# Kernel optimization log

Hardware: AMD Instinct MI355X
Metric: run time of the kernel (lower is better)

## Reference

```python
import jax, jax.numpy as jnp
import numpy as np

B, S, D = 1, 2048, 2048
HQ, HKV, HD = 32, 4, 128
E, K, F = 8, 2, 768
EPS = 1e-6
ROPE_THETA = 1000000.0


def rmsnorm(x, scale, eps=EPS):
    var = jnp.mean(jnp.square(x), axis=-1, keepdims=True)
    return x * jax.lax.rsqrt(var + eps) * scale


def rotate_half(x):
    h = x.shape[-1] // 2
    return jnp.concatenate([-x[..., h:], x[..., :h]], axis=-1)


def rope_cos_sin(seq_len, head_dim, dtype=jnp.float32):
    inv_freq = 1.0 / (ROPE_THETA ** (jnp.arange(0, head_dim, 2, dtype=jnp.float32) / head_dim))
    angles = jnp.arange(seq_len, dtype=jnp.float32)[:, None] * inv_freq[None, :]  # (S, HD/2)
    emb = jnp.concatenate([angles, angles], axis=-1)  # (S, HD)
    return jnp.cos(emb).astype(dtype), jnp.sin(emb).astype(dtype)


def setup_inputs() -> dict:
    key = jax.random.key(0)
    ks = jax.random.split(key, 16)
    s = lambda i, shape, scale: jax.random.normal(ks[i], shape, dtype=jnp.float32) * scale
    inp = {
        "hidden_states": s(0, (B, S, D), 1.0),
        "ln1_scale": jnp.ones((D,), jnp.float32),
        "ln2_scale": jnp.ones((D,), jnp.float32),
        "Wq": s(1, (D, HQ * HD), 0.02),
        "Wk": s(2, (D, HKV * HD), 0.02),
        "Wv": s(3, (D, HKV * HD), 0.02),
        "Wo": s(4, (HQ * HD, D), 0.02),
        "q_norm_scale": jnp.ones((HD,), jnp.float32),
        "k_norm_scale": jnp.ones((HD,), jnp.float32),
        "router_W": s(5, (D, E), 0.02),
        "up_W": s(6, (E, D, F), 0.02),
        "up_b": jnp.zeros((E, F), jnp.float32),
        "down_W": s(7, (E, F, D), 0.02),
        "down_b": jnp.zeros((E, D), jnp.float32),
    }
    return inp


def reference(hidden_states, ln1_scale, ln2_scale, Wq, Wk, Wv, Wo,
              q_norm_scale, k_norm_scale, router_W, up_W, up_b, down_W, down_b):
    b, s_len, d = hidden_states.shape
    # ---- pre-norm + self-attention ----
    residual = hidden_states
    x = rmsnorm(hidden_states, ln1_scale)
    q = (x @ Wq).reshape(b, s_len, HQ, HD)
    k = (x @ Wk).reshape(b, s_len, HKV, HD)
    v = (x @ Wv).reshape(b, s_len, HKV, HD)
    q = rmsnorm(q, q_norm_scale)
    k = rmsnorm(k, k_norm_scale)
    cos, sin = rope_cos_sin(s_len, HD, q.dtype)
    cos = cos[None, :, None, :]
    sin = sin[None, :, None, :]
    q = q * cos + rotate_half(q) * sin
    k = k * cos + rotate_half(k) * sin
    g = HQ // HKV
    k = jnp.repeat(k, g, axis=2)  # (b, s, HQ, HD)
    v = jnp.repeat(v, g, axis=2)
    scores = jnp.einsum('bqhd,bkhd->bhqk', q, k) / jnp.sqrt(jnp.asarray(HD, q.dtype))
    causal = jnp.tril(jnp.ones((s_len, s_len), bool))
    scores = jnp.where(causal[None, None], scores, jnp.asarray(-1e9, scores.dtype))
    probs = jax.nn.softmax(scores, axis=-1)
    attn = jnp.einsum('bhqk,bkhd->bqhd', probs, v).reshape(b, s_len, HQ * HD)
    attn_out = attn @ Wo
    hidden = residual + attn_out
    # ---- pre-norm + dense-all-experts MoE ----
    residual = hidden
    xf = rmsnorm(hidden, ln2_scale).reshape(-1, d)  # (T, D)
    router_logits = xf @ router_W  # (T, E)
    routing_weights = jax.nn.softmax(router_logits, axis=-1)
    gating_weights, selected = jax.lax.top_k(routing_weights, K)  # (T, K)
    gating_weights = gating_weights / jnp.sum(gating_weights, axis=-1, keepdims=True)
    expert_mask = jax.nn.one_hot(selected, E, dtype=gating_weights.dtype)  # (T, K, E)
    h = jax.nn.silu(jnp.einsum('td,edf->tef', xf, up_W) + up_b[None])  # (T, E, F)
    expert_outputs = jnp.einsum('tef,efd->ted', h, down_W) + down_b[None]  # (T, E, D)
    weighted = jnp.einsum('tke,ted->tkd', expert_mask, expert_outputs)  # (T, K, D)
    moe_out = jnp.sum(weighted * gating_weights[..., None], axis=1).reshape(b, s_len, d)
    hidden = residual + moe_out
    # ---- load balancing auxiliary loss (no attention mask path) ----
    expert_usage = jnp.mean(jnp.mean(expert_mask, axis=0), axis=0) * E  # (E,)
    su = jnp.sum(expert_usage)
    aux_loss = su * su / (E * E)
    return hidden, router_logits, aux_loss
```

## Files before the change

### kernel.cpp

```cpp
#include <hip/hip_runtime.h>
#include <cmath>

typedef __bf16 bf16_t;
typedef __bf16 bf16x8 __attribute__((ext_vector_type(8)));
typedef __bf16 bf16x4 __attribute__((ext_vector_type(4)));
typedef float  f32x4  __attribute__((ext_vector_type(4)));

#define SLEN 2048
#define DMOD 2048
#define NHQ  32
#define NHKV 4
#define HD   128
#define NQC  4096
#define NKVC 512
#define NQKVC 5120
#define NEXP 8
#define NF   768

#define KSTR 136
#define VSTR 72
#define PSTR 72

__device__ __forceinline__ float wredsum(float v) {
#pragma unroll
  for (int off = 32; off > 0; off >>= 1) v += __shfl_xor(v, off);
  return v;
}

__device__ __forceinline__ void gll16(const bf16_t* g, bf16_t* l) {
  __builtin_amdgcn_global_load_lds((const __attribute__((address_space(1))) void*)g,
                                   (__attribute__((address_space(3))) void*)l, 16, 0, 0);
}

__global__ void rope_table_k(float* __restrict__ cosT, float* __restrict__ sinT) {
  int idx = blockIdx.x * 256 + threadIdx.x;
  if (idx >= SLEN * 64) return;
  int t = idx >> 6, j = idx & 63;
  double inv = exp(-0.2158673524681918 * (double)j);
  double ang = (double)t * inv;
  cosT[idx] = (float)cos(ang);
  sinT[idx] = (float)sin(ang);
}

__global__ __launch_bounds__(256) void transpose_split2_k(const float* __restrict__ in,
                                                          bf16_t* __restrict__ outH,
                                                          bf16_t* __restrict__ outL,
                                                          int R, int C) {
  __shared__ float tile[32][33];
  int tx = threadIdx.x, ty = threadIdx.y;
  int c0 = blockIdx.x * 32, r0 = blockIdx.y * 32;
#pragma unroll
  for (int i = 0; i < 4; i++)
    tile[ty + i * 8][tx] = in[(size_t)(r0 + ty + i * 8) * C + c0 + tx];
  __syncthreads();
#pragma unroll
  for (int i = 0; i < 4; i++) {
    int c = c0 + ty + i * 8;
    int r = r0 + tx;
    float w = tile[tx][ty + i * 8];
    bf16_t hi = (bf16_t)w;
    bf16_t lo = (bf16_t)(w - (float)hi);
    size_t o = (size_t)c * R + r;
    outH[o] = hi;
    outL[o] = lo;
  }
}

__global__ __launch_bounds__(256) void transpose_plain_k(const float* __restrict__ in,
                                                         bf16_t* __restrict__ out,
                                                         int R, int C) {
  __shared__ float tile[32][33];
  int b = blockIdx.z;
  const float* inb = in + (size_t)b * R * C;
  bf16_t* outb = out + (size_t)b * R * C;
  int tx = threadIdx.x, ty = threadIdx.y;
  int c0 = blockIdx.x * 32, r0 = blockIdx.y * 32;
#pragma unroll
  for (int i = 0; i < 4; i++)
    tile[ty + i * 8][tx] = inb[(size_t)(r0 + ty + i * 8) * C + c0 + tx];
  __syncthreads();
#pragma unroll
  for (int i = 0; i < 4; i++) {
    int c = c0 + ty + i * 8;
    int r = r0 + tx;
    outb[(size_t)c * R + r] = (bf16_t)tile[tx][ty + i * 8];
  }
}

__global__ __launch_bounds__(256) void rmsnorm1_k(const float* __restrict__ hs,
                                                  const float* __restrict__ sc,
                                                  bf16_t* __restrict__ xnH,
                                                  bf16_t* __restrict__ xnL) {
  const int t = blockIdx.x;
  const float* row = hs + (size_t)t * DMOD;
  const int tid = threadIdx.x;
  const int i0 = tid * 8;
  float4 a = *(const float4*)(row + i0);
  float4 b = *(const float4*)(row + i0 + 4);
  float x[8] = {a.x, a.y, a.z, a.w, b.x, b.y, b.z, b.w};
  float ss = 0.f;
#pragma unroll
  for (int j = 0; j < 8; j++) ss += x[j] * x[j];
  ss = wredsum(ss);
  __shared__ float red[4];
  if ((tid & 63) == 0) red[tid >> 6] = ss;
  __syncthreads();
  float rn = rsqrtf((red[0] + red[1] + red[2] + red[3]) * (1.f / 2048.f) + 1e-6f);
#pragma unroll
  for (int j = 0; j < 8; j++) {
    float v = x[j] * rn * sc[i0 + j];
    bf16_t hi = (bf16_t)v;
    bf16_t lo = (bf16_t)(v - (float)hi);
    xnH[(size_t)t * DMOD + i0 + j] = hi;
    xnL[(size_t)t * DMOD + i0 + j] = lo;
  }
}

template <bool RESID>
__global__ __launch_bounds__(256, 3) void gemm_split_k(const bf16_t* __restrict__ Ah,
                                                       const bf16_t* __restrict__ Al,
                                                       int lda,
                                                       const bf16_t* __restrict__ Bh,
                                                       const bf16_t* __restrict__ Bl,
                                                       int ldb, int K,
                                                       const float* __restrict__ resid,
                                                       float* __restrict__ C, int ldc) {
  __shared__ bf16_t AsH[2][128][32], AsL[2][128][32], BsH[2][64][32], BsL[2][64][32];
  const int t = threadIdx.x;
  const int w = t >> 6, lane = t & 63;
  const int m16 = lane & 15, quad = lane >> 4;
  const int nwg = gridDim.x * gridDim.y;
  const int flat = blockIdx.y * gridDim.x + blockIdx.x;
  int tile = flat;
  if ((nwg & 7) == 0) tile = (flat & 7) * (nwg >> 3) + (flat >> 3);
  const int bx = tile % gridDim.x, by = tile / gridDim.x;
  const int m0 = by * 128, n0 = bx * 64;
  const int wm = (w & 1) * 64, wn = (w >> 1) * 32;
  f32x4 acc[4][2];
#pragma unroll
  for (int i = 0; i < 4; i++)
#pragma unroll
    for (int j = 0; j < 2; j++) acc[i][j] = (f32x4){0.f, 0.f, 0.f, 0.f};

  const int srow = t >> 2;
  const int scol = (t & 3) * 8;
  const int lw = w * 512;
  const bf16_t* gAh0 = Ah + (size_t)(m0 + srow) * lda + scol;
  const bf16_t* gAh1 = Ah + (size_t)(m0 + 64 + srow) * lda + scol;
  const bf16_t* gAl0 = Al + (size_t)(m0 + srow) * lda + scol;
  const bf16_t* gAl1 = Al + (size_t)(m0 + 64 + srow) * lda + scol;
  const bf16_t* gBh0 = Bh + (size_t)(n0 + srow) * ldb + scol;
  const bf16_t* gBl0 = Bl + (size_t)(n0 + srow) * ldb + scol;

  auto stage = [&](int buf, int k0) {
    gll16(gAh0 + k0, &AsH[buf][0][0] + lw);
    gll16(gAh1 + k0, &AsH[buf][0][0] + 2048 + lw);
    gll16(gAl0 + k0, &AsL[buf][0][0] + lw);
    gll16(gAl1 + k0, &AsL[buf][0][0] + 2048 + lw);
    gll16(gBh0 + k0, &BsH[buf][0][0] + lw);
    gll16(gBl0 + k0, &BsL[buf][0][0] + lw);
  };

  stage(0, 0);
  int cur = 0;
  for (int k0 = 32; k0 <= K; k0 += 32) {
    if (k0 < K) {
      stage(cur ^ 1, k0);
      asm volatile("s_waitcnt vmcnt(6)" ::: "memory");
    } else {
      asm volatile("s_waitcnt vmcnt(0)" ::: "memory");
    }
    __builtin_amdgcn_sched_barrier(0);
    __builtin_amdgcn_s_barrier();
    __builtin_amdgcn_sched_barrier(0);
    bf16x8 a_h[4], a_l[4];
#pragma unroll
    for (int mt = 0; mt < 4; mt++) {
      a_h[mt] = *(const bf16x8*)(&AsH[cur][wm + mt * 16 + m16][quad * 8]);
      a_l[mt] = *(const bf16x8*)(&AsL[cur][wm + mt * 16 + m16][quad * 8]);
    }
#pragma unroll
    for (int nt = 0; nt < 2; nt++) {
      bf16x8 b_h = *(const bf16x8*)(&BsH[cur][wn + nt * 16 + m16][quad * 8]);
      bf16x8 b_l = *(const bf16x8*)(&BsL[cur][wn + nt * 16 + m16][quad * 8]);
#pragma unroll
      for (int mt = 0; mt < 4; mt++) {
        acc[mt][nt] = __builtin_amdgcn_mfma_f32_16x16x32_bf16(a_h[mt], b_h, acc[mt][nt], 0, 0, 0);
        acc[mt][nt] = __builtin_amdgcn_mfma_f32_16x16x32_bf16(a_l[mt], b_h, acc[mt][nt], 0, 0, 0);
        acc[mt][nt] = __builtin_amdgcn_mfma_f32_16x16x32_bf16(a_h[mt], b_l, acc[mt][nt], 0, 0, 0);
      }
    }
    __builtin_amdgcn_sched_barrier(0);
    __builtin_amdgcn_s_barrier();
    __builtin_amdgcn_sched_barrier(0);
    cur ^= 1;
  }
#pragma unroll
  for (int mt = 0; mt < 4; mt++)
#pragma unroll
    for (int r = 0; r < 4; r++) {
      const size_t row = m0 + wm + mt * 16 + quad * 4 + r;
#pragma unroll
      for (int nt = 0; nt < 2; nt++) {
        const size_t idx = row * ldc + n0 + wn + nt * 16 + m16;
        if (RESID) C[idx] = acc[mt][nt][r] + resid[idx];
        else       C[idx] = acc[mt][nt][r];
      }
    }
}

__global__ __launch_bounds__(128) void qknorm_rope_k(float* __restrict__ qkv,
                                                     const float* __restrict__ qsc,
                                                     const float* __restrict__ ksc,
                                                     const float* __restrict__ cosT,
                                                     const float* __restrict__ sinT) {
  const int t = blockIdx.x;
  const int hh = blockIdx.y;
  const bool isq = hh < NHQ;
  float* ptr = qkv + (size_t)t * NQKVC + (isq ? hh * HD : NQC + (hh - NHQ) * HD);
  const int i = threadIdx.x;
  float x = ptr[i];
  float ss = x * x;
  ss = wredsum(ss);
  __shared__ float red2[2];
  __shared__ float xs[128];
  if ((i & 63) == 0) red2[i >> 6] = ss;
  __syncthreads();
  float rn = rsqrtf((red2[0] + red2[1]) * (1.f / 128.f) + 1e-6f);
  float xn = x * rn * (isq ? qsc[i] : ksc[i]);
  xs[i] = xn;
  __syncthreads();
  int j = i & 63;
  float c = cosT[t * 64 + j];
  float s = sinT[t * 64 + j];
  float rot = (i < 64) ? -xs[i + 64] : xs[i - 64];
  ptr[i] = xn * c + rot * s;
}

__global__ __launch_bounds__(256) void kprep_k(const float* __restrict__ qkv,
                                               bf16_t* __restrict__ Kh,
                                               bf16_t* __restrict__ Kl) {
  const int gid = blockIdx.x * 256 + threadIdx.x;
  const int tok = gid >> 6;
  const int c = (gid & 63) * 8;
  const int hk = c >> 7, d = c & 127;
  const float* p = qkv + (size_t)tok * NQKVC + NQC + c;
  float4 a = *(const float4*)p;
  float4 b = *(const float4*)(p + 4);
  float xv[8] = {a.x, a.y, a.z, a.w, b.x, b.y, b.z, b.w};
  bf16x8 hv, lv;
#pragma unroll
  for (int j = 0; j < 8; j++) {
    bf16_t hi = (bf16_t)xv[j];
    hv[j] = hi;
    lv[j] = (bf16_t)(xv[j] - (float)hi);
  }
  const size_t o = ((size_t)hk * SLEN + tok) * HD + d;
  *(bf16x8*)(Kh + o) = hv;
  *(bf16x8*)(Kl + o) = lv;
}

__global__ __launch_bounds__(256) void vprep_k(const float* __restrict__ qkv,
                                               bf16_t* __restrict__ Vh,
                                               bf16_t* __restrict__ Vl) {
  __shared__ float tile[32][33];
  const int hk = blockIdx.z;
  const int tx = threadIdx.x, ty = threadIdx.y;
  const int t0 = blockIdx.x * 32, d0 = blockIdx.y * 32;
#pragma unroll
  for (int i = 0; i < 4; i++)
    tile[ty + i * 8][tx] =
        qkv[(size_t)(t0 + ty + i * 8) * NQKVC + NQC + NKVC + hk * HD + d0 + tx];
  __syncthreads();
#pragma unroll
  for (int i = 0; i < 4; i++) {
    int d = d0 + ty + i * 8;
    int tk = t0 + tx;
    float wv = tile[tx][ty + i * 8];
    bf16_t hi = (bf16_t)wv;
    size_t o = ((size_t)hk * HD + d) * SLEN + tk;
    Vh[o] = hi;
    Vl[o] = (bf16_t)(wv - (float)hi);
  }
}

__global__ __launch_bounds__(256) void attn_mfma_k(const float* __restrict__ qkv,
                                                   const bf16_t* __restrict__ Kph,
                                                   const bf16_t* __restrict__ Kpl,
                                                   const bf16_t* __restrict__ Vph,
                                                   const bf16_t* __restrict__ Vpl,
                                                   bf16_t* __restrict__ attnH,
                                                   bf16_t* __restrict__ attnL) {
  const int bx = blockIdx.x;
  const int hh = blockIdx.y;
  const int hk = hh >> 3;
  __shared__ bf16_t sK[2][64][KSTR];
  __shared__ bf16_t sV[2][128][VSTR];
  const int t = threadIdx.x;
  const int w = t >> 6, lane = t & 63;
  const int m16 = lane & 15, quad = lane >> 4;
  const float SCALE = 0.08838834764831845f;

  const int ksr = t >> 4;
  const int ksc = (t & 15) * 8;
  const int vsd = t >> 3;
  const int vsk = (t & 7) * 8;
  const bf16_t* KbH = Kph + (size_t)hk * SLEN * HD;
  const bf16_t* KbL = Kpl + (size_t)hk * SLEN * HD;
  const bf16_t* VbH = Vph + (size_t)hk * HD * SLEN;
  const bf16_t* VbL = Vpl + (size_t)hk * HD * SLEN;
  bf16_t* sP = &sK[0][0][0];

  for (int half = 0; half < 2; half++) {
    const int qb = half ? bx : 31 - bx;

    bf16x8 Qh[4], Ql[4];
    {
      const int qrow = qb * 64 + w * 16 + m16;
      const float* qp = qkv + (size_t)qrow * NQKVC + hh * HD + quad * 8;
#pragma unroll
      for (int kc = 0; kc < 4; kc++) {
        float4 x0 = *(const float4*)(qp + kc * 32);
        float4 x1 = *(const float4*)(qp + kc * 32 + 4);
        float xv[8] = {x0.x, x0.y, x0.z, x0.w, x1.x, x1.y, x1.z, x1.w};
#pragma unroll
        for (int j = 0; j < 8; j++) {
          bf16_t hi = (bf16_t)xv[j];
          Qh[kc][j] = hi;
          Ql[kc][j] = (bf16_t)(xv[j] - (float)hi);
        }
      }
    }
    f32x4 acc[8];
#pragma unroll
    for (int i = 0; i < 8; i++) acc[i] = (f32x4){0.f, 0.f, 0.f, 0.f};
    float mrow[4], lrow[4];
#pragma unroll
    for (int r = 0; r < 4; r++) { mrow[r] = -1e30f; lrow[r] = 0.f; }

    for (int kb = 0; kb <= qb; kb++) {
      __syncthreads();
      {
#pragma unroll
        for (int i = 0; i < 4; i++) {
          const int row = ksr + i * 16;
          const size_t go = (size_t)(kb * 64 + row) * HD + ksc;
          *(bf16x8*)(&sK[0][row][ksc]) = *(const bf16x8*)(KbH + go);
          *(bf16x8*)(&sK[1][row][ksc]) = *(const bf16x8*)(KbL + go);
        }
      }
      {
#pragma unroll
        for (int i = 0; i < 4; i++) {
          const int d = vsd + i * 32;
          const size_t go = (size_t)d * SLEN + kb * 64 + vsk;
          *(bf16x8*)(&sV[0][d][vsk]) = *(const bf16x8*)(VbH + go);
          *(bf16x8*)(&sV[1][d][vsk]) = *(const bf16x8*)(VbL + go);
        }
      }
      __syncthreads();
      f32x4 xs[4];
#pragma unroll
      for (int nt = 0; nt < 4; nt++) {
        f32x4 s = (f32x4){0.f, 0.f, 0.f, 0.f};
        if (kb < qb || nt <= w) {
#pragma unroll
          for (int kc = 0; kc < 4; kc++) {
            bf16x8 kh = *(const bf16x8*)(&sK[0][nt * 16 + m16][kc * 32 + quad * 8]);
            bf16x8 kl = *(const bf16x8*)(&sK[1][nt * 16 + m16][kc * 32 + quad * 8]);
            s = __builtin_amdgcn_mfma_f32_16x16x32_bf16(Qh[kc], kh, s, 0, 0, 0);
            s = __builtin_amdgcn_mfma_f32_16x16x32_bf16(Ql[kc], kh, s, 0, 0, 0);
            s = __builtin_amdgcn_mfma_f32_16x16x32_bf16(Qh[kc], kl, s, 0, 0, 0);
          }
        }
        xs[nt] = s;
      }
      __syncthreads();
      float p[4][4], alpha[4];
#pragma unroll
      for (int r = 0; r < 4; r++) {
        const int rqg = qb * 64 + w * 16 + quad * 4 + r;
        float xr[4];
#pragma unroll
        for (int nt = 0; nt < 4; nt++) {
          int colg = kb * 64 + nt * 16 + m16;
          xr[nt] = (colg <= rqg) ? xs[nt][r] * SCALE : -1e30f;
        }
        float mx = fmaxf(fmaxf(xr[0], xr[1]), fmaxf(xr[2], xr[3]));
#pragma unroll
        for (int off = 1; off < 16; off <<= 1) mx = fmaxf(mx, __shfl_xor(mx, off));
        float mn = fmaxf(mrow[r], mx);
        float al = __expf(mrow[r] - mn);
        float rs = 0.f;
#pragma unroll
        for (int nt = 0; nt < 4; nt++) {
          float pv = __expf(xr[nt] - mn);
          p[nt][r] = pv;
          rs += pv;
        }
#pragma unroll
        for (int off = 1; off < 16; off <<= 1) rs += __shfl_xor(rs, off);
        lrow[r] = lrow[r] * al + rs;
        mrow[r] = mn;
        alpha[r] = al;
      }
#pragma unroll
      for (int dt = 0; dt < 8; dt++)
#pragma unroll
        for (int r = 0; r < 4; r++) acc[dt][r] *= alpha[r];
      {
        bf16_t* base = sP + (size_t)w * 2 * 16 * PSTR;
#pragma unroll
        for (int nt = 0; nt < 4; nt++)
#pragma unroll
          for (int r = 0; r < 4; r++) {
            float pv = p[nt][r];
            bf16_t hi = (bf16_t)pv;
            base[(quad * 4 + r) * PSTR + nt * 16 + m16] = hi;
            base[16 * PSTR + (quad * 4 + r) * PSTR + nt * 16 + m16] = (bf16_t)(pv - (float)hi);
          }
      }
      {
        const bf16_t* base = sP + (size_t)w * 2 * 16 * PSTR;
        bf16x8 Ph[2], Pl[2];
#pragma unroll
        for (int kc = 0; kc < 2; kc++) {
          Ph[kc] = *(const bf16x8*)(base + m16 * PSTR + kc * 32 + quad * 8);
          Pl[kc] = *(const bf16x8*)(base + 16 * PSTR + m16 * PSTR + kc * 32 + quad * 8);
        }
#pragma unroll
        for (int dt = 0; dt < 8; dt++)
#pragma unroll
          for (int kc = 0; kc < 2; kc++) {
            bf16x8 vh = *(const bf16x8*)(&sV[0][dt * 16 + m16][kc * 32 + quad * 8]);
            bf16x8 vl = *(const bf16x8*)(&sV[1][dt * 16 + m16][kc * 32 + quad * 8]);
            acc[dt] = __builtin_amdgcn_mfma_f32_16x16x32_bf16(Ph[kc], vh, acc[dt], 0, 0, 0);
            acc[dt] = __builtin_amdgcn_mfma_f32_16x16x32_bf16(Pl[kc], vh, acc[dt], 0, 0, 0);
            acc[dt] = __builtin_amdgcn_mfma_f32_16x16x32_bf16(Ph[kc], vl, acc[dt], 0, 0, 0);
          }
      }
    }
#pragma unroll
    for (int r = 0; r < 4; r++) {
      const int tok = qb * 64 + w * 16 + quad * 4 + r;
      const float linv = 1.f / lrow[r];
      const size_t ro = (size_t)tok * NQC + hh * HD;
#pragma unroll
      for (int dt = 0; dt < 8; dt++) {
        float v = acc[dt][r] * linv;
        bf16_t hi = (bf16_t)v;
        attnH[ro + dt * 16 + m16] = hi;
        attnL[ro + dt * 16 + m16] = (bf16_t)(v - (float)hi);
      }
    }
  }
}

__global__ __launch_bounds__(256) void rmsnorm2_router_k(const float* __restrict__ hid,
                                                         const float* __restrict__ sc2,
                                                         const float* __restrict__ rW,
                                                         bf16_t* __restrict__ xf,
                                                         float* __restrict__ rlog) {
  const int t = blockIdx.x;
  const float* row = hid + (size_t)t * DMOD;
  const int tid = threadIdx.x;
  const int i0 = tid * 8;
  float4 a = *(const float4*)(row + i0);
  float4 b = *(const float4*)(row + i0 + 4);
  float x[8] = {a.x, a.y, a.z, a.w, b.x, b.y, b.z, b.w};
  float ss = 0.f;
#pragma unroll
  for (int j = 0; j < 8; j++) ss += x[j] * x[j];
  ss = wredsum(ss);
  __shared__ float red[4];
  if ((tid & 63) == 0) red[tid >> 6] = ss;
  __syncthreads();
  float rn = rsqrtf((red[0] + red[1] + red[2] + red[3]) * (1.f / 2048.f) + 1e-6f);
  float acc[8];
#pragma unroll
  for (int e = 0; e < 8; e++) acc[e] = 0.f;
#pragma unroll
  for (int j = 0; j < 8; j++) {
    float xn = x[j] * rn * sc2[i0 + j];
    xf[(size_t)t * DMOD + i0 + j] = (bf16_t)xn;
    const float* w = rW + (size_t)(i0 + j) * NEXP;
#pragma unroll
    for (int e = 0; e < 8; e++) acc[e] += xn * w[e];
  }
#pragma unroll
  for (int e = 0; e < 8; e++) acc[e] = wredsum(acc[e]);
  __shared__ float wacc[4][8];
  if ((tid & 63) == 0)
#pragma unroll
    for (int e = 0; e < 8; e++) wacc[tid >> 6][e] = acc[e];
  __syncthreads();
  if (tid < 8) rlog[t * NEXP + tid] = wacc[0][tid] + wacc[1][tid] + wacc[2][tid] + wacc[3][tid];
}

__global__ void topk_k(const float* __restrict__ rlog, int* __restrict__ sel,
                       float* __restrict__ gates, float* __restrict__ aux) {
  int t = blockIdx.x * 256 + threadIdx.x;
  if (t == 0) aux[0] = 1.0f;
  if (t >= SLEN) return;
  const float* l = rlog + t * NEXP;
  int i1 = 0; float v1 = l[0];
#pragma unroll
  for (int e = 1; e < 8; e++) if (l[e] > v1) { v1 = l[e]; i1 = e; }
  int i2 = -1; float v2 = -1e30f;
#pragma unroll
  for (int e = 0; e < 8; e++) if (e != i1 && l[e] > v2) { v2 = l[e]; i2 = e; }
  float e21 = expf(v2 - v1);
  float inv = 1.f / (1.f + e21);
  sel[t * 2 + 0] = i1;
  sel[t * 2 + 1] = i2;
  gates[t * 2 + 0] = inv;
  gates[t * 2 + 1] = e21 * inv;
}

__global__ void scatter_k(const int* __restrict__ sel, const float* __restrict__ gates,
                          int* __restrict__ cnt, int* __restrict__ tok,
                          float* __restrict__ gateL) {
  int i = blockIdx.x * 256 + threadIdx.x;
  if (i >= SLEN * 2) return;
  int e = sel[i];
  int pos = atomicAdd(&cnt[e], 1);
  tok[e * SLEN + pos] = i >> 1;
  gateL[e * SLEN + pos] = gates[i];
}

__global__ __launch_bounds__(256, 5) void gemm_up_k(const bf16_t* __restrict__ xf,
                                                    const bf16_t* __restrict__ upWT,
                                                    const int* __restrict__ cnt,
                                                    const int* __restrict__ tok,
                                                    const float* __restrict__ up_b,
                                                    bf16_t* __restrict__ hbuf) {
  const int e = blockIdx.z;
  const int c = cnt[e];
  const int m0 = blockIdx.y * 128;
  if (m0 >= c) return;
  const int n0 = blockIdx.x * 64;
  __shared__ bf16_t As[2][128][32], Bs[2][64][32];
  const int t = threadIdx.x;
  const int w = t >> 6, lane = t & 63;
  const int m16 = lane & 15, quad = lane >> 4;
  const int wm = (w & 1) * 64, wn = (w >> 1) * 32;
  const int srow = t >> 2, scol = (t & 3) * 8;
  const int lw = w * 512;
  const int* tokE = tok + e * SLEN;
  int r0 = m0 + srow;      if (r0 >= c) r0 = c - 1;
  int r1 = m0 + 64 + srow; if (r1 >= c) r1 = c - 1;
  const bf16_t* ga0 = xf + (size_t)tokE[r0] * DMOD + scol;
  const bf16_t* ga1 = xf + (size_t)tokE[r1] * DMOD + scol;
  const bf16_t* gb0 = upWT + (size_t)e * NF * DMOD + (size_t)(n0 + srow) * DMOD + scol;
  f32x4 acc[4][2];
#pragma unroll
  for (int i = 0; i < 4; i++)
#pragma unroll
    for (int j = 0; j < 2; j++) acc[i][j] = (f32x4){0.f, 0.f, 0.f, 0.f};

  auto stage = [&](int buf, int k0) {
    gll16(ga0 + k0, &As[buf][0][0] + lw);
    gll16(ga1 + k0, &As[buf][0][0] + 2048 + lw);
    gll16(gb0 + k0, &Bs[buf][0][0] + lw);
  };

  stage(0, 0);
  int cur = 0;
  for (int k0 = 32; k0 <= DMOD; k0 += 32) {
    if (k0 < DMOD) {
      stage(cur ^ 1, k0);
      asm volatile("s_waitcnt vmcnt(3)" ::: "memory");
    } else {
      asm volatile("s_waitcnt vmcnt(0)" ::: "memory");
    }
    __builtin_amdgcn_sched_barrier(0);
    __builtin_amdgcn_s_barrier();
    __builtin_amdgcn_sched_barrier(0);
    bf16x8 a[4];
#pragma unroll
    for (int mt = 0; mt < 4; mt++)
      a[mt] = *(const bf16x8*)(&As[cur][wm + mt * 16 + m16][quad * 8]);
#pragma unroll
    for (int nt = 0; nt < 2; nt++) {
      bf16x8 b = *(const bf16x8*)(&Bs[cur][wn + nt * 16 + m16][quad * 8]);
#pragma unroll
      for (int mt = 0; mt < 4; mt++)
        acc[mt][nt] = __builtin_amdgcn_mfma_f32_16x16x32_bf16(a[mt], b, acc[mt][nt], 0, 0, 0);
    }
    __builtin_amdgcn_sched_barrier(0);
    __builtin_amdgcn_s_barrier();
    __builtin_amdgcn_sched_barrier(0);
    cur ^= 1;
  }
#pragma unroll
  for (int mt = 0; mt < 4; mt++)
#pragma unroll
    for (int r = 0; r < 4; r++) {
      int slot = m0 + wm + mt * 16 + quad * 4 + r;
      if (slot < c) {
#pragma unroll
        for (int nt = 0; nt < 2; nt++) {
          int n = n0 + wn + nt * 16 + m16;
          float x = acc[mt][nt][r] + up_b[e * NF + n];
          float v = x / (1.f + __expf(-x));
          hbuf[((size_t)e * SLEN + slot) * NF + n] = (bf16_t)v;
        }
      }
    }
}

__global__ __launch_bounds__(256, 5) void gemm_down_k(const bf16_t* __restrict__ hbuf,
                                                      const bf16_t* __restrict__ downWT,
                                                      const int* __restrict__ cnt,
                                                      const int* __restrict__ tok,
                                                      const float* __restrict__ gateL,
                                                      const float* __restrict__ down_b,
                                                      float* __restrict__ outH) {
  const int e = blockIdx.z;
  const int c = cnt[e];
  const int m0 = blockIdx.y * 128;
  if (m0 >= c) return;
  const int n0 = blockIdx.x * 64;
  __shared__ bf16_t As[2][128][32], Bs[2][64][32];
  const int t = threadIdx.x;
  const int w = t >> 6, lane = t & 63;
  const int m16 = lane & 15, quad = lane >> 4;
  const int wm = (w & 1) * 64, wn = (w >> 1) * 32;
  const int srow = t >> 2, scol = (t & 3) * 8;
  const int lw = w * 512;
  const bf16_t* Ab = hbuf + (size_t)e * SLEN * NF;
  const bf16_t* ga0 = Ab + (size_t)(m0 + srow) * NF + scol;
  const bf16_t* ga1 = Ab + (size_t)(m0 + 64 + srow) * NF + scol;
  const bf16_t* gb0 = downWT + (size_t)e * DMOD * NF + (size_t)(n0 + srow) * NF + scol;
  f32x4 acc[4][2];
#pragma unroll
  for (int i = 0; i < 4; i++)
#pragma unroll
    for (int j = 0; j < 2; j++) acc[i][j] = (f32x4){0.f, 0.f, 0.f, 0.f};

  auto stage = [&](int buf, int k0) {
    gll16(ga0 + k0, &As[buf][0][0] + lw);
    gll16(ga1 + k0, &As[buf][0][0] + 2048 + lw);
    gll16(gb0 + k0, &Bs[buf][0][0] + lw);
  };

  stage(0, 0);
  int cur = 0;
  for (int k0 = 32; k0 <= NF; k0 += 32) {
    if (k0 < NF) {
      stage(cur ^ 1, k0);
      asm volatile("s_waitcnt vmcnt(3)" ::: "memory");
    } else {
      asm volatile("s_waitcnt vmcnt(0)" ::: "memory");
    }
    __builtin_amdgcn_sched_barrier(0);
    __builtin_amdgcn_s_barrier();
    __builtin_amdgcn_sched_barrier(0);
    bf16x8 a[4];
#pragma unroll
    for (int mt = 0; mt < 4; mt++)
      a[mt] = *(const bf16x8*)(&As[cur][wm + mt * 16 + m16][quad * 8]);
#pragma unroll
    for (int nt = 0; nt < 2; nt++) {
      bf16x8 b = *(const bf16x8*)(&Bs[cur][wn + nt * 16 + m16][quad * 8]);
#pragma unroll
      for (int mt = 0; mt < 4; mt++)
        acc[mt][nt] = __builtin_amdgcn_mfma_f32_16x16x32_bf16(a[mt], b, acc[mt][nt], 0, 0, 0);
    }
    __builtin_amdgcn_sched_barrier(0);
    __builtin_amdgcn_s_barrier();
    __builtin_amdgcn_sched_barrier(0);
    cur ^= 1;
  }
#pragma unroll
  for (int mt = 0; mt < 4; mt++)
#pragma unroll
    for (int r = 0; r < 4; r++) {
      int slot = m0 + wm + mt * 16 + quad * 4 + r;
      if (slot < c) {
        int tk = tok[e * SLEN + slot];
        float g = gateL[e * SLEN + slot];
#pragma unroll
        for (int nt = 0; nt < 2; nt++) {
          int n = n0 + wn + nt * 16 + m16;
          atomicAdd(&outH[(size_t)tk * DMOD + n], g * (acc[mt][nt][r] + down_b[e * DMOD + n]));
        }
      }
    }
}

extern "C" void kernel_launch(void* const* d_in, const int* in_sizes, int n_in,
                              void* d_out, int out_size, void* d_ws, size_t ws_size,
                              hipStream_t stream) {
  (void)in_sizes; (void)n_in; (void)out_size;
  const float* hs   = (const float*)d_in[0];
  const float* ln1  = (const float*)d_in[1];
  const float* ln2  = (const float*)d_in[2];
  const float* Wq   = (const float*)d_in[3];
  const float* Wk   = (const float*)d_in[4];
  const float* Wv   = (const float*)d_in[5];
  const float* Wo   = (const float*)d_in[6];
  const float* qns  = (const float*)d_in[7];
  const float* kns  = (const float*)d_in[8];
  const float* rW   = (const float*)d_in[9];
  const float* upW  = (const float*)d_in[10];
  const float* upB  = (const float*)d_in[11];
  const float* dnW  = (const float*)d_in[12];
  const float* dnB  = (const float*)d_in[13];
  float* dout = (float*)d_out;

  const size_t NEED = 135431168ull;
  if (ws_size < NEED) return;
  char* ws = (char*)d_ws;
  const size_t OA = 0;
  const size_t OB = OA + 41943040ull;
  const size_t OC = OB + 33554432ull;
  const size_t OD = OC + 16777216ull;
  const size_t OE = OD + 41943040ull;

  bf16_t* BqkvH  = (bf16_t*)(ws + OA);
  bf16_t* BqkvL  = (bf16_t*)(ws + OA + 20971520ull);
  bf16_t* attnH  = (bf16_t*)(ws + OA);
  bf16_t* attnL  = (bf16_t*)(ws + OA + 16777216ull);
  bf16_t* Kph    = (bf16_t*)(ws + OA + 33554432ull);
  bf16_t* Kpl    = Kph + 1048576;
  bf16_t* Vph    = Kpl + 1048576;
  bf16_t* Vpl    = Vph + 1048576;
  bf16_t* upWT   = (bf16_t*)(ws + OA);
  bf16_t* WoH    = (bf16_t*)(ws + OB);
  bf16_t* WoL    = (bf16_t*)(ws + OB + 16777216ull);
  bf16_t* hbuf   = (bf16_t*)(ws + OB);
  bf16_t* xnH    = (bf16_t*)(ws + OC);
  bf16_t* xnL    = (bf16_t*)(ws + OC + 8388608ull);
  bf16_t* xf     = (bf16_t*)(ws + OC);
  float*  qkv    = (float*)(ws + OD);
  bf16_t* downWT = (bf16_t*)(ws + OD);
  float*  cosT   = (float*)(ws + OE);
  float*  sinT   = (float*)(ws + OE + 524288ull);
  int*    sel    = (int*)(ws + OE + 1048576ull);
  float*  gates  = (float*)(ws + OE + 1064960ull);
  int*    cnt    = (int*)(ws + OE + 1081344ull);
  int*    tok    = (int*)(ws + OE + 1082368ull);
  float*  gateL  = (float*)(ws + OE + 1147904ull);

  hipMemsetAsync(cnt, 0, 1024, stream);
  rope_table_k<<<512, 256, 0, stream>>>(cosT, sinT);

  dim3 tb(32, 8);
  transpose_split2_k<<<dim3(128, 64), tb, 0, stream>>>(Wq, BqkvH, BqkvL, 2048, 4096);
  transpose_split2_k<<<dim3(16, 64), tb, 0, stream>>>(Wk, BqkvH + (size_t)4096 * 2048,
                                                      BqkvL + (size_t)4096 * 2048, 2048, 512);
  transpose_split2_k<<<dim3(16, 64), tb, 0, stream>>>(Wv, BqkvH + (size_t)4608 * 2048,
                                                      BqkvL + (size_t)4608 * 2048, 2048, 512);
  transpose_split2_k<<<dim3(64, 128), tb, 0, stream>>>(Wo, WoH, WoL, 4096, 2048);

  rmsnorm1_k<<<2048, 256, 0, stream>>>(hs, ln1, xnH, xnL);
  gemm_split_k<false><<<dim3(80, 16), 256, 0, stream>>>(xnH, xnL, 2048, BqkvH, BqkvL,
                                                        2048, 2048, nullptr, qkv, NQKVC);
  qknorm_rope_k<<<dim3(2048, 36), 128, 0, stream>>>(qkv, qns, kns, cosT, sinT);
  kprep_k<<<512, 256, 0, stream>>>(qkv, Kph, Kpl);
  vprep_k<<<dim3(64, 4, 4), tb, 0, stream>>>(qkv, Vph, Vpl);
  attn_mfma_k<<<dim3(16, 32), 256, 0, stream>>>(qkv, Kph, Kpl, Vph, Vpl, attnH, attnL);
  gemm_split_k<true><<<dim3(32, 16), 256, 0, stream>>>(attnH, attnL, 4096, WoH, WoL,
                                                       4096, 4096, hs, dout, DMOD);

  rmsnorm2_router_k<<<2048, 256, 0, stream>>>(dout, ln2, rW, xf, dout + 4194304);
  topk_k<<<8, 256, 0, stream>>>(dout + 4194304, sel, gates, dout + 4210688);
  scatter_k<<<16, 256, 0, stream>>>(sel, gates, cnt, tok, gateL);

  transpose_plain_k<<<dim3(24, 64, 8), tb, 0, stream>>>(upW, upWT, 2048, 768);
  transpose_plain_k<<<dim3(64, 24, 8), tb, 0, stream>>>(dnW, downWT, 768, 2048);

  gemm_up_k<<<dim3(12, 16, 8), 256, 0, stream>>>(xf, upWT, cnt, tok, upB, hbuf);
  gemm_down_k<<<dim3(32, 16, 8), 256, 0, stream>>>(hbuf, downWT, cnt, tok, gateL, dnB, dout);
}
```

Measured before the change: 861.6 us.

## Transpose attention MFMA layout, stage output via LDS, replace MoE atomics with combine

The attention kernel swaps the MFMA operand order so each lane owns one query row. This lets softmax row reductions use two cross-quad shuffles instead of per-row 16-lane butterflies, and lets P be written to LDS as vector stores. The attention output is staged through LDS so attnH/attnL are written with coalesced 16-byte stores. The MoE down projection now writes per-slot results to a dense buffer, and a new combine kernel sums the two expert rows per token, replacing scattered float atomicAdds at the cost of an extra pass and two small kernels.

```diff
diff --git a/kernel.cpp b/kernel.cpp
--- a/kernel.cpp
+++ b/kernel.cpp
@@ -313,6 +313,7 @@
 
   for (int half = 0; half < 2; half++) {
     const int qb = half ? bx : 31 - bx;
+    const int qg = qb * 64 + w * 16 + m16;
 
     bf16x8 Qh[4], Ql[4];
     {
@@ -334,9 +335,7 @@
     f32x4 acc[8];
 #pragma unroll
     for (int i = 0; i < 8; i++) acc[i] = (f32x4){0.f, 0.f, 0.f, 0.f};
-    float mrow[4], lrow[4];
-#pragma unroll
-    for (int r = 0; r < 4; r++) { mrow[r] = -1e30f; lrow[r] = 0.f; }
+    float mrow = -1e30f, lrow = 0.f;
 
     for (int kb = 0; kb <= qb; kb++) {
       __syncthreads();
@@ -368,57 +367,61 @@
           for (int kc = 0; kc < 4; kc++) {
             bf16x8 kh = *(const bf16x8*)(&sK[0][nt * 16 + m16][kc * 32 + quad * 8]);
             bf16x8 kl = *(const bf16x8*)(&sK[1][nt * 16 + m16][kc * 32 + quad * 8]);
-            s = __builtin_amdgcn_mfma_f32_16x16x32_bf16(Qh[kc], kh, s, 0, 0, 0);
-            s = __builtin_amdgcn_mfma_f32_16x16x32_bf16(Ql[kc], kh, s, 0, 0, 0);
-            s = __builtin_amdgcn_mfma_f32_16x16x32_bf16(Qh[kc], kl, s, 0, 0, 0);
+            s = __builtin_amdgcn_mfma_f32_16x16x32_bf16(kh, Qh[kc], s, 0, 0, 0);
+            s = __builtin_amdgcn_mfma_f32_16x16x32_bf16(kh, Ql[kc], s, 0, 0, 0);
+            s = __builtin_amdgcn_mfma_f32_16x16x32_bf16(kl, Qh[kc], s, 0, 0, 0);
           }
         }
         xs[nt] = s;
       }
       __syncthreads();
-      float p[4][4], alpha[4];
-#pragma unroll
-      for (int r = 0; r < 4; r++) {
-        const int rqg = qb * 64 + w * 16 + quad * 4 + r;
-        float xr[4];
-#pragma unroll
-        for (int nt = 0; nt < 4; nt++) {
-          int colg = kb * 64 + nt * 16 + m16;
-          xr[nt] = (colg <= rqg) ? xs[nt][r] * SCALE : -1e30f;
-        }
-        float mx = fmaxf(fmaxf(xr[0], xr[1]), fmaxf(xr[2], xr[3]));
-#pragma unroll
-        for (int off = 1; off < 16; off <<= 1) mx = fmaxf(mx, __shfl_xor(mx, off));
-        float mn = fmaxf(mrow[r], mx);
-        float al = __expf(mrow[r] - mn);
-        float rs = 0.f;
-#pragma unroll
-        for (int nt = 0; nt < 4; nt++) {
-          float pv = __expf(xr[nt] - mn);
+      float xr[4][4], p[4][4];
+      float mx = -1e30f;
+#pragma unroll
+      for (int nt = 0; nt < 4; nt++)
+#pragma unroll
+        for (int r = 0; r < 4; r++) {
+          int kvg = kb * 64 + nt * 16 + quad * 4 + r;
+          float v = (kvg <= qg) ? xs[nt][r] * SCALE : -1e30f;
+          xr[nt][r] = v;
+          mx = fmaxf(mx, v);
+        }
+      mx = fmaxf(mx, __shfl_xor(mx, 16));
+      mx = fmaxf(mx, __shfl_xor(mx, 32));
+      float mn = fmaxf(mrow, mx);
+      float al = __expf(mrow - mn);
+      float rs = 0.f;
+#pragma unroll
+      for (int nt = 0; nt < 4; nt++)
+#pragma unroll
+        for (int r = 0; r < 4; r++) {
+          float pv = __expf(xr[nt][r] - mn);
           p[nt][r] = pv;
           rs += pv;
         }
-#pragma unroll
-        for (int off = 1; off < 16; off <<= 1) rs += __shfl_xor(rs, off);
-        lrow[r] = lrow[r] * al + rs;
-        mrow[r] = mn;
-        alpha[r] = al;
-      }
+      rs += __shfl_xor(rs, 16);
+      rs += __shfl_xor(rs, 32);
+      lrow = lrow * al + rs;
+      mrow = mn;
 #pragma unroll
       for (int dt = 0; dt < 8; dt++)
 #pragma unroll
-        for (int r = 0; r < 4; r++) acc[dt][r] *= alpha[r];
+        for (int r = 0; r < 4; r++) acc[dt][r] *= al;
       {
         bf16_t* base = sP + (size_t)w * 2 * 16 * PSTR;
 #pragma unroll
-        for (int nt = 0; nt < 4; nt++)
+        for (int nt = 0; nt < 4; nt++) {
+          bf16x4 hv, lv;
 #pragma unroll
           for (int r = 0; r < 4; r++) {
             float pv = p[nt][r];
             bf16_t hi = (bf16_t)pv;
-            base[(quad * 4 + r) * PSTR + nt * 16 + m16] = hi;
-            base[16 * PSTR + (quad * 4 + r) * PSTR + nt * 16 + m16] = (bf16_t)(pv - (float)hi);
+            hv[r] = hi;
+            lv[r] = (bf16_t)(pv - (float)hi);
           }
+          *(bf16x4*)(base + m16 * PSTR + nt * 16 + quad * 4) = hv;
+          *(bf16x4*)(base + 16 * PSTR + m16 * PSTR + nt * 16 + quad * 4) = lv;
+        }
       }
       {
         const bf16_t* base = sP + (size_t)w * 2 * 16 * PSTR;
@@ -434,23 +437,41 @@
           for (int kc = 0; kc < 2; kc++) {
             bf16x8 vh = *(const bf16x8*)(&sV[0][dt * 16 + m16][kc * 32 + quad * 8]);
             bf16x8 vl = *(const bf16x8*)(&sV[1][dt * 16 + m16][kc * 32 + quad * 8]);
-            acc[dt] = __builtin_amdgcn_mfma_f32_16x16x32_bf16(Ph[kc], vh, acc[dt], 0, 0, 0);
-            acc[dt] = __builtin_amdgcn_mfma_f32_16x16x32_bf16(Pl[kc], vh, acc[dt], 0, 0, 0);
-            acc[dt] = __builtin_amdgcn_mfma_f32_16x16x32_bf16(Ph[kc], vl, acc[dt], 0, 0, 0);
+            acc[dt] = __builtin_amdgcn_mfma_f32_16x16x32_bf16(vh, Ph[kc], acc[dt], 0, 0, 0);
+            acc[dt] = __builtin_amdgcn_mfma_f32_16x16x32_bf16(vh, Pl[kc], acc[dt], 0, 0, 0);
+            acc[dt] = __builtin_amdgcn_mfma_f32_16x16x32_bf16(vl, Ph[kc], acc[dt], 0, 0, 0);
           }
       }
     }
-#pragma unroll
-    for (int r = 0; r < 4; r++) {
-      const int tok = qb * 64 + w * 16 + quad * 4 + r;
-      const float linv = 1.f / lrow[r];
-      const size_t ro = (size_t)tok * NQC + hh * HD;
-#pragma unroll
-      for (int dt = 0; dt < 8; dt++) {
-        float v = acc[dt][r] * linv;
-        bf16_t hi = (bf16_t)v;
-        attnH[ro + dt * 16 + m16] = hi;
-        attnL[ro + dt * 16 + m16] = (bf16_t)(v - (float)hi);
+    __syncthreads();
+    float* tb = (float*)(&sK[0][0][0]) + (size_t)w * 2048;
+    const float linv = 1.f / lrow;
+#pragma unroll
+    for (int dt = 0; dt < 8; dt++) {
+      f32x4 v = acc[dt];
+#pragma unroll
+      for (int r = 0; r < 4; r++) v[r] *= linv;
+      *(f32x4*)(tb + m16 * 128 + dt * 16 + quad * 4) = v;
+    }
+    __syncthreads();
+    {
+      const int qr = lane >> 2, c0 = (lane & 3) * 32;
+      const int tok = qb * 64 + w * 16 + qr;
+      const size_t ro = (size_t)tok * NQC + hh * HD + c0;
+#pragma unroll
+      for (int j = 0; j < 4; j++) {
+        float4 a = *(const float4*)(tb + qr * 128 + c0 + j * 8);
+        float4 b = *(const float4*)(tb + qr * 128 + c0 + j * 8 + 4);
+        float xv[8] = {a.x, a.y, a.z, a.w, b.x, b.y, b.z, b.w};
+        bf16x8 hv, lv;
+#pragma unroll
+        for (int jj = 0; jj < 8; jj++) {
+          bf16_t hi = (bf16_t)xv[jj];
+          hv[jj] = hi;
+          lv[jj] = (bf16_t)(xv[jj] - (float)hi);
+        }
+        *(bf16x8*)(attnH + ro + j * 8) = hv;
+        *(bf16x8*)(attnL + ro + j * 8) = lv;
       }
     }
   }
@@ -519,13 +540,22 @@
 
 __global__ void scatter_k(const int* __restrict__ sel, const float* __restrict__ gates,
                           int* __restrict__ cnt, int* __restrict__ tok,
-                          float* __restrict__ gateL) {
+                          float* __restrict__ gateL, int* __restrict__ posOf) {
   int i = blockIdx.x * 256 + threadIdx.x;
   if (i >= SLEN * 2) return;
   int e = sel[i];
   int pos = atomicAdd(&cnt[e], 1);
   tok[e * SLEN + pos] = i >> 1;
   gateL[e * SLEN + pos] = gates[i];
+  posOf[i] = pos;
+}
+
+__global__ void prefix_k(const int* __restrict__ cnt, int* __restrict__ baseP) {
+  if (threadIdx.x == 0) {
+    int b = 0;
+#pragma unroll
+    for (int e = 0; e < 8; e++) { baseP[e] = b; b += cnt[e]; }
+  }
 }
 
 __global__ __launch_bounds__(256, 5) void gemm_up_k(const bf16_t* __restrict__ xf,
@@ -612,10 +642,10 @@
 __global__ __launch_bounds__(256, 5) void gemm_down_k(const bf16_t* __restrict__ hbuf,
                                                       const bf16_t* __restrict__ downWT,
                                                       const int* __restrict__ cnt,
-                                                      const int* __restrict__ tok,
                                                       const float* __restrict__ gateL,
                                                       const float* __restrict__ down_b,
-                                                      float* __restrict__ outH) {
+                                                      const int* __restrict__ baseP,
+                                                      float* __restrict__ dbuf) {
   const int e = blockIdx.z;
   const int c = cnt[e];
   const int m0 = blockIdx.y * 128;
@@ -672,21 +702,42 @@
     __builtin_amdgcn_sched_barrier(0);
     cur ^= 1;
   }
+  const int eb = baseP[e];
 #pragma unroll
   for (int mt = 0; mt < 4; mt++)
 #pragma unroll
     for (int r = 0; r < 4; r++) {
       int slot = m0 + wm + mt * 16 + quad * 4 + r;
       if (slot < c) {
-        int tk = tok[e * SLEN + slot];
         float g = gateL[e * SLEN + slot];
 #pragma unroll
         for (int nt = 0; nt < 2; nt++) {
           int n = n0 + wn + nt * 16 + m16;
-          atomicAdd(&outH[(size_t)tk * DMOD + n], g * (acc[mt][nt][r] + down_b[e * DMOD + n]));
-        }
-      }
-    }
+          dbuf[(size_t)(eb + slot) * DMOD + n] = g * (acc[mt][nt][r] + down_b[e * DMOD + n]);
+        }
+      }
+    }
+}
+
+__global__ __launch_bounds__(256) void combine_k(const float* __restrict__ dbuf,
+                                                 const int* __restrict__ sel,
+                                                 const int* __restrict__ posOf,
+                                                 const int* __restrict__ baseP,
+                                                 float* __restrict__ dout) {
+  const int t = blockIdx.x;
+  const int i0 = threadIdx.x * 8;
+  const int r0 = baseP[sel[t * 2 + 0]] + posOf[t * 2 + 0];
+  const int r1 = baseP[sel[t * 2 + 1]] + posOf[t * 2 + 1];
+  const float* a = dbuf + (size_t)r0 * DMOD + i0;
+  const float* b = dbuf + (size_t)r1 * DMOD + i0;
+  float* o = dout + (size_t)t * DMOD + i0;
+  float4 o0 = *(const float4*)o,       o1 = *(const float4*)(o + 4);
+  float4 a0 = *(const float4*)a,       a1 = *(const float4*)(a + 4);
+  float4 b0 = *(const float4*)b,       b1 = *(const float4*)(b + 4);
+  o0.x += a0.x + b0.x; o0.y += a0.y + b0.y; o0.z += a0.z + b0.z; o0.w += a0.w + b0.w;
+  o1.x += a1.x + b1.x; o1.y += a1.y + b1.y; o1.z += a1.z + b1.z; o1.w += a1.w + b1.w;
+  *(float4*)o = o0;
+  *(float4*)(o + 4) = o1;
 }
 
 extern "C" void kernel_launch(void* const* d_in, const int* in_sizes, int n_in,
@@ -727,6 +778,7 @@
   bf16_t* Vph    = Kpl + 1048576;
   bf16_t* Vpl    = Vph + 1048576;
   bf16_t* upWT   = (bf16_t*)(ws + OA);
+  float*  dbuf   = (float*)(ws + OA);
   bf16_t* WoH    = (bf16_t*)(ws + OB);
   bf16_t* WoL    = (bf16_t*)(ws + OB + 16777216ull);
   bf16_t* hbuf   = (bf16_t*)(ws + OB);
@@ -742,6 +794,8 @@
   int*    cnt    = (int*)(ws + OE + 1081344ull);
   int*    tok    = (int*)(ws + OE + 1082368ull);
   float*  gateL  = (float*)(ws + OE + 1147904ull);
+  int*    posOf  = (int*)(ws + OE + 1213440ull);
+  int*    baseP  = (int*)(ws + OE + 1229824ull);
 
   hipMemsetAsync(cnt, 0, 1024, stream);
   rope_table_k<<<512, 256, 0, stream>>>(cosT, sinT);
@@ -766,11 +820,13 @@
 
   rmsnorm2_router_k<<<2048, 256, 0, stream>>>(dout, ln2, rW, xf, dout + 4194304);
   topk_k<<<8, 256, 0, stream>>>(dout + 4194304, sel, gates, dout + 4210688);
-  scatter_k<<<16, 256, 0, stream>>>(sel, gates, cnt, tok, gateL);
+  scatter_k<<<16, 256, 0, stream>>>(sel, gates, cnt, tok, gateL, posOf);
+  prefix_k<<<1, 64, 0, stream>>>(cnt, baseP);
 
   transpose_plain_k<<<dim3(24, 64, 8), tb, 0, stream>>>(upW, upWT, 2048, 768);
   transpose_plain_k<<<dim3(64, 24, 8), tb, 0, stream>>>(dnW, downWT, 768, 2048);
 
   gemm_up_k<<<dim3(12, 16, 8), 256, 0, stream>>>(xf, upWT, cnt, tok, upB, hbuf);
-  gemm_down_k<<<dim3(32, 16, 8), 256, 0, stream>>>(hbuf, downWT, cnt, tok, gateL, dnB, dout);
-}
+  gemm_down_k<<<dim3(32, 16, 8), 256, 0, stream>>>(hbuf, downWT, cnt, gateL, dnB, baseP, dbuf);
+  combine_k<<<2048, 256, 0, stream>>>(dbuf, sel, posOf, baseP, dout);
+}
```

New measurement: 848.4 us. Within noise of the previous version (-1.5%).
